# Performance work log

Hardware: AMD Instinct MI355X
Metric: run time of the kernel (lower is better)

The kernel has to match this reference:

```python
import jax, jax.numpy as jnp
import numpy as np

B, C, V, L = 32, 32, 1024, 13  # batch, channels, nodes, seq_len
SUPPORT_LEN, ORDER = 3, 2
C_IN_TOTAL = (ORDER * SUPPORT_LEN + 1) * C  # 224
C_OUT = 64


def setup_inputs() -> dict:
    key = jax.random.key(0)
    ks = jax.random.split(key, 6)
    x = jax.random.normal(ks[0], (B, C, V, L), dtype=jnp.float32)
    # row-normalized random adjacencies (dense diffusion matrices)
    def adj(k):
        a = jax.random.uniform(k, (V, V), dtype=jnp.float32)
        return a / jnp.sum(a, axis=1, keepdims=True)
    A0, A1, A2 = adj(ks[1]), adj(ks[2]), adj(ks[3])
    W = jax.random.normal(ks[4], (C_OUT, C_IN_TOTAL), dtype=jnp.float32) * (1.0 / np.sqrt(C_IN_TOTAL))
    b = jnp.zeros((C_OUT,), dtype=jnp.float32)
    return {"x": x, "A0": A0, "A1": A1, "A2": A2, "W": W, "b": b}


def nconv(x, A):
    # x: [b, c, v, l], A: [v, w] -> [b, c, w, l]
    return jnp.einsum('bcvl,vw->bcwl', x, A)


def reference(x, A0, A1, A2, W, b):
    out = [x]
    for A in (A0, A1, A2):
        x1 = nconv(x, A)
        out.append(x1)
        for _ in range(2, ORDER + 1):
            x2 = nconv(x1, A)
            out.append(x2)
            x1 = x2
    h = jnp.concatenate(out, axis=1)  # [b, (order*support_len+1)*c, v, l]
    # 1x1 conv == channel contraction; dropout is identity in eval mode
    return jnp.einsum('bcvl,oc->bovl', h, W) + b[None, :, None, None]
```

## Files before the change

### kernel.cpp

```cpp
#include <hip/hip_runtime.h>
#include <hip/hip_bf16.h>
#include <cstdint>


#define SZE 13631488ull
#define OFF_AT  190840832ull
#define OFF_WB  197132288ull
#define WS_NEED 197160960ull

typedef __attribute__((ext_vector_type(8))) short short8;
typedef __attribute__((ext_vector_type(4))) float f32x4;

__device__ __forceinline__ unsigned short f2b(float f) {
    unsigned int u = __builtin_bit_cast(unsigned int, f);
    u += 0x7FFFu + ((u >> 16) & 1u);
    return (unsigned short)(u >> 16);
}

__device__ __forceinline__ void gl2lds16(const unsigned short* g, unsigned short* l) {
    __builtin_amdgcn_global_load_lds(
        (__attribute__((address_space(1))) void*)(g),
        (__attribute__((address_space(3))) void*)(l), 16, 0, 0);
}

__global__ __launch_bounds__(256) void k_prep(const float* __restrict__ x,
                                              unsigned short* __restrict__ T,
                                              unsigned short* __restrict__ Ht) {
    __shared__ unsigned short sb[32 * 840];
    const int b = blockIdx.x >> 4, vc = blockIdx.x & 15;
    const int t = threadIdx.x;
    const float4* xb = (const float4*)x;
    for (int it = 0; it < 26; ++it) {
        int q = it * 256 + t;
        int c = q / 208, f = q - c * 208;
        float4 u = xb[(size_t)(b * 32 + c) * 3328 + vc * 208 + f];
        ushort4 pk; pk.x = f2b(u.x); pk.y = f2b(u.y); pk.z = f2b(u.z); pk.w = f2b(u.w);
        *(ushort4*)(sb + c * 840 + f * 4) = pk;
    }
    __syncthreads();
    unsigned short* Tb = T + (size_t)b * 13 * 32 * 1024 + (size_t)vc * 64;
    for (int it = 0; it < 26; ++it) {
        int q = it * 256 + t;
        int l = q >> 9, r = q & 511, c = r >> 4, sg = r & 15;
        const unsigned short* src = sb + c * 840 + l;
        ushort4 pk;
        pk.x = src[(sg * 4 + 0) * 13];
        pk.y = src[(sg * 4 + 1) * 13];
        pk.z = src[(sg * 4 + 2) * 13];
        pk.w = src[(sg * 4 + 3) * 13];
        *(ushort4*)(Tb + (size_t)(l * 32 + c) * 1024 + sg * 4) = pk;
    }
    unsigned short* Hb = Ht + ((size_t)b * 13312 + (size_t)vc * 832) * 224;
    for (int it = 0; it < 26; ++it) {
        int q = it * 256 + t;
        int v = q / 104, r = q - v * 104, l = r >> 3, cs = r & 7;
        const unsigned short* src = sb + v * 13 + l;
        ushort4 pk;
        pk.x = src[(cs * 4 + 0) * 840];
        pk.y = src[(cs * 4 + 1) * 840];
        pk.z = src[(cs * 4 + 2) * 840];
        pk.w = src[(cs * 4 + 3) * 840];
        *(ushort4*)(Hb + (size_t)(v * 13 + l) * 224 + cs * 4) = pk;
    }
}

__global__ __launch_bounds__(256) void k_prep_A(const float* __restrict__ A0,
                                                const float* __restrict__ A1,
                                                const float* __restrict__ A2,
                                                unsigned short* __restrict__ AT) {
    const float* A = blockIdx.z == 0 ? A0 : blockIdx.z == 1 ? A1 : A2;
    unsigned short* D = AT + (size_t)blockIdx.z * 1024 * 1024;
    __shared__ float tile[32][33];
    int v0 = blockIdx.y * 32, w0 = blockIdx.x * 32;
    int c = threadIdx.x & 31, r = threadIdx.x >> 5;
    for (int p = 0; p < 4; ++p) {
        int rr = r + p * 8;
        tile[rr][c] = A[(size_t)(v0 + rr) * 1024 + w0 + c];
    }
    __syncthreads();
    for (int p = 0; p < 4; ++p) {
        int rr = r + p * 8;
        D[(size_t)(w0 + rr) * 1024 + v0 + c] = f2b(tile[c][rr]);
    }
}

__global__ __launch_bounds__(256) void k_prep_W(const float* __restrict__ W,
                                                unsigned short* __restrict__ Wb) {
    int idx = blockIdx.x * 256 + threadIdx.x;
    Wb[idx] = f2b(W[idx]);
}

__global__ __launch_bounds__(256) void k_gemm(const unsigned short* __restrict__ Xb, long xz,
                                              const unsigned short* __restrict__ Pb,
                                              unsigned short* __restrict__ Tout, long tz,
                                              unsigned short* __restrict__ Ht, int cc0b,
                                              int doT) {
    __shared__ union {
        struct { unsigned short xs[8192]; unsigned short ps[8192]; } s;
        unsigned short cs[128 * 132];
        unsigned short ct[128 * 136];
    } lds;
    const int z = blockIdx.z;
    const unsigned short* X = Xb + (size_t)z * (size_t)xz;
    const unsigned short* P = Pb + (size_t)z * (1024u * 1024u);
    const int i0 = blockIdx.x * 128;
    const int j0 = blockIdx.y * 128;
    const int t = threadIdx.x;
    const int lane = t & 63, wave = t >> 6;
    const int l16 = lane & 15, quad = lane >> 4;
    const int wi = (wave >> 1) * 64, wj = (wave & 1) * 64;

    f32x4 acc[4][4] = {};

    const int row = t >> 2, seg = t & 3;
    const unsigned short* xg0 = X + (size_t)(i0 + row) * 1024 + seg * 8;
    const unsigned short* xg1 = xg0 + (size_t)64 * 1024;
    const unsigned short* pg0 = P + (size_t)(j0 + row) * 1024 + seg * 8;
    const unsigned short* pg1 = pg0 + (size_t)64 * 1024;
    unsigned short* lx0 = lds.s.xs + t * 8;
    unsigned short* lp0 = lds.s.ps + t * 8;

    for (int kt = 0; kt < 16; ++kt) {
        const int ko = kt * 64;
        gl2lds16(xg0 + ko,      lx0);
        gl2lds16(xg1 + ko,      lx0 + 2048);
        gl2lds16(xg0 + ko + 32, lx0 + 4096);
        gl2lds16(xg1 + ko + 32, lx0 + 6144);
        gl2lds16(pg0 + ko,      lp0);
        gl2lds16(pg1 + ko,      lp0 + 2048);
        gl2lds16(pg0 + ko + 32, lp0 + 4096);
        gl2lds16(pg1 + ko + 32, lp0 + 6144);
        __syncthreads();
#pragma unroll
        for (int p = 0; p < 2; ++p) {
            short8 a[4], b[4];
#pragma unroll
            for (int mi = 0; mi < 4; ++mi)
                a[mi] = *(const short8*)(lds.s.xs + p * 4096 + (wi + mi * 16 + l16) * 32 + quad * 8);
#pragma unroll
            for (int nj = 0; nj < 4; ++nj)
                b[nj] = *(const short8*)(lds.s.ps + p * 4096 + (wj + nj * 16 + l16) * 32 + quad * 8);
#pragma unroll
            for (int mi = 0; mi < 4; ++mi)
#pragma unroll
                for (int nj = 0; nj < 4; ++nj)
                    acc[mi][nj] = __builtin_amdgcn_mfma_f32_16x16x32_bf16(a[mi], b[nj], acc[mi][nj], 0, 0, 0);
        }
        __syncthreads();
    }

    if (doT) {
#pragma unroll
        for (int mi = 0; mi < 4; ++mi)
#pragma unroll
            for (int nj = 0; nj < 4; ++nj)
#pragma unroll
                for (int r = 0; r < 4; ++r)
                    lds.cs[(wi + mi * 16 + quad * 4 + r) * 132 + (wj + nj * 16 + l16)] =
                        f2b(acc[mi][nj][r]);
        __syncthreads();
        unsigned short* O = Tout + (size_t)z * (size_t)tz;
#pragma unroll
        for (int rep = 0; rep < 8; ++rep) {
            int q = rep * 256 + t;
            int rr = q >> 4, sg = q & 15;
            *(uint4*)(O + (size_t)(i0 + rr) * 1024 + j0 + sg * 8) =
                *(const uint4*)(lds.cs + rr * 132 + sg * 8);
        }
        __syncthreads();
    }

#pragma unroll
    for (int mi = 0; mi < 4; ++mi)
#pragma unroll
        for (int nj = 0; nj < 4; ++nj) {
            ushort4 pk;
            pk.x = f2b(acc[mi][nj][0]);
            pk.y = f2b(acc[mi][nj][1]);
            pk.z = f2b(acc[mi][nj][2]);
            pk.w = f2b(acc[mi][nj][3]);
            *(ushort4*)(lds.ct + (wj + nj * 16 + l16) * 136 + wi + mi * 16 + quad * 4) = pk;
        }
    __syncthreads();
    const int cc0 = cc0b + 64 * z;
#pragma unroll
    for (int it = 0; it < 8; ++it) {
        int q = it * 256 + t;
        int sg = q & 3, v = (q >> 2) & 127, s = q >> 9;
        int p = (i0 >> 5) + s;
        int b = p / 13, l = p - b * 13;
        size_t m = (size_t)b * 13312 + (size_t)(j0 + v) * 13 + l;
        *(uint4*)(Ht + m * 224 + cc0 + sg * 8) =
            *(const uint4*)(lds.ct + v * 136 + s * 32 + sg * 8);
    }
}

__global__ __launch_bounds__(256) void k_fc(const unsigned short* __restrict__ Ht,
                                            const unsigned short* __restrict__ Wb,
                                            const float* __restrict__ bias,
                                            float* __restrict__ y) {
    __shared__ union {
        struct { unsigned short w[64 * 232]; unsigned short a[208 * 32]; } s;
        float sy[64 * 212];
    } lds;
    const int bid = blockIdx.x;
    const int b = bid >> 6, v0 = (bid & 63) * 16;
    const size_t m0 = (size_t)b * 13312 + (size_t)v0 * 13;
    const int t = threadIdx.x;
    const int lane = t & 63, wave = t >> 6;
    const int l16 = lane & 15, quad = lane >> 4;
    const int o0 = wave * 16;

    for (int it = 0; it < 7; ++it) {
        int q = it * 256 + t;
        int o = q / 28, sg = q % 28;
        *(uint4*)(lds.s.w + o * 232 + sg * 8) = *(const uint4*)(Wb + o * 224 + sg * 8);
    }
    float bv = bias[o0 + l16];
    f32x4 acc[13];
#pragma unroll
    for (int mf = 0; mf < 13; ++mf) acc[mf] = (f32x4){bv, bv, bv, bv};

    for (int kk = 0; kk < 7; ++kk) {
        __syncthreads();
        for (int it = 0; it < 4; ++it) {
            int q = it * 256 + t;
            if (q < 832)
                gl2lds16(Ht + (m0 + (q >> 2)) * 224 + kk * 32 + (q & 3) * 8,
                         lds.s.a + q * 8);
        }
        __syncthreads();
        short8 bf = *(const short8*)(lds.s.w + (o0 + l16) * 232 + kk * 32 + quad * 8);
#pragma unroll
        for (int mf = 0; mf < 13; ++mf) {
            short8 af = *(const short8*)(lds.s.a + (mf * 16 + l16) * 32 + quad * 8);
            acc[mf] = __builtin_amdgcn_mfma_f32_16x16x32_bf16(af, bf, acc[mf], 0, 0, 0);
        }
    }
    __syncthreads();
#pragma unroll
    for (int mf = 0; mf < 13; ++mf)
#pragma unroll
        for (int r = 0; r < 4; ++r)
            lds.sy[(o0 + l16) * 212 + mf * 16 + quad * 4 + r] = acc[mf][r];
    __syncthreads();
    float* yb = y + (size_t)b * 851968 + (size_t)v0 * 13;
    for (int it = 0; it < 13; ++it) {
        int q = it * 256 + t;
        int o = q / 52, sg = q % 52;
        *(float4*)(yb + (size_t)o * 13312 + sg * 4) = *(const float4*)(lds.sy + o * 212 + sg * 4);
    }
}

extern "C" void kernel_launch(void* const* d_in, const int* in_sizes, int n_in,
                              void* d_out, int out_size, void* d_ws, size_t ws_size,
                              hipStream_t stream) {
    const float* x    = (const float*)d_in[0];
    const float* A0   = (const float*)d_in[1];
    const float* A1   = (const float*)d_in[2];
    const float* A2   = (const float*)d_in[3];
    const float* W    = (const float*)d_in[4];
    const float* bias = (const float*)d_in[5];

    if (ws_size < WS_NEED) return;

    unsigned short* Ht = (unsigned short*)d_ws;
    unsigned short* AT = (unsigned short*)((char*)d_ws + OFF_AT);
    unsigned short* Wb = (unsigned short*)((char*)d_ws + OFF_WB);
    unsigned short* Tarena = (unsigned short*)d_out;

    k_prep<<<512, 256, 0, stream>>>(x, Tarena, Ht);
    k_prep_A<<<dim3(32, 32, 3), 256, 0, stream>>>(A0, A1, A2, AT);
    k_prep_W<<<56, 256, 0, stream>>>(W, Wb);
    k_gemm<<<dim3(104, 8, 3), 256, 0, stream>>>(Tarena, 0L, AT,
                                                Tarena + SZE, (long)SZE, Ht, 32, 1);
    k_gemm<<<dim3(104, 8, 3), 256, 0, stream>>>(Tarena + SZE, (long)SZE, AT,
                                                nullptr, 0L, Ht, 64, 0);
    k_fc<<<2048, 256, 0, stream>>>(Ht, Wb, bias, (float*)d_out);
}
```

Measured before the change: 508.6 us.

## Precompute squared adjacency A·A and compute all six diffusions in one GEMM launch

Instead of chaining x·A then (x·A)·A, the code first computes the 1024x1024 squared adjacency matrices with a small GEMM. It then runs a single GEMM launch over six z-slices, covering x·A and x·A² for each support, so the dependent second large GEMM over the activations is gone. The squared matrix is rounded to bf16 before use, which changes numerics slightly. The fc kernel is also restructured into 128-thread blocks that keep the activation fragments in registers with next-tile prefetch and write outputs directly, removing the LDS staging.

```diff
diff --git a/kernel.cpp b/kernel.cpp
--- a/kernel.cpp
+++ b/kernel.cpp
@@ -67,15 +67,19 @@
 __global__ __launch_bounds__(256) void k_prep_A(const float* __restrict__ A0,
                                                 const float* __restrict__ A1,
                                                 const float* __restrict__ A2,
-                                                unsigned short* __restrict__ AT) {
+                                                unsigned short* __restrict__ AT,
+                                                unsigned short* __restrict__ Abf) {
     const float* A = blockIdx.z == 0 ? A0 : blockIdx.z == 1 ? A1 : A2;
     unsigned short* D = AT + (size_t)blockIdx.z * 1024 * 1024;
+    unsigned short* D2 = Abf + (size_t)blockIdx.z * 1024 * 1024;
     __shared__ float tile[32][33];
     int v0 = blockIdx.y * 32, w0 = blockIdx.x * 32;
     int c = threadIdx.x & 31, r = threadIdx.x >> 5;
     for (int p = 0; p < 4; ++p) {
         int rr = r + p * 8;
-        tile[rr][c] = A[(size_t)(v0 + rr) * 1024 + w0 + c];
+        float val = A[(size_t)(v0 + rr) * 1024 + w0 + c];
+        tile[rr][c] = val;
+        D2[(size_t)(v0 + rr) * 1024 + w0 + c] = f2b(val);
     }
     __syncthreads();
     for (int p = 0; p < 4; ++p) {
@@ -91,10 +95,10 @@
 }
 
 __global__ __launch_bounds__(256) void k_gemm(const unsigned short* __restrict__ Xb, long xz,
-                                              const unsigned short* __restrict__ Pb,
+                                              const unsigned short* __restrict__ P0,
+                                              const unsigned short* __restrict__ P1,
                                               unsigned short* __restrict__ Tout, long tz,
-                                              unsigned short* __restrict__ Ht, int cc0b,
-                                              int doT) {
+                                              unsigned short* __restrict__ Ht, int doT) {
     __shared__ union {
         struct { unsigned short xs[8192]; unsigned short ps[8192]; } s;
         unsigned short cs[128 * 132];
@@ -102,7 +106,8 @@
     } lds;
     const int z = blockIdx.z;
     const unsigned short* X = Xb + (size_t)z * (size_t)xz;
-    const unsigned short* P = Pb + (size_t)z * (1024u * 1024u);
+    const unsigned short* P = (z < 3) ? P0 + (size_t)z * 1048576u
+                                      : P1 + (size_t)(z - 3) * 1048576u;
     const int i0 = blockIdx.x * 128;
     const int j0 = blockIdx.y * 128;
     const int t = threadIdx.x;
@@ -170,85 +175,86 @@
         __syncthreads();
     }
 
-#pragma unroll
-    for (int mi = 0; mi < 4; ++mi)
-#pragma unroll
-        for (int nj = 0; nj < 4; ++nj) {
-            ushort4 pk;
-            pk.x = f2b(acc[mi][nj][0]);
-            pk.y = f2b(acc[mi][nj][1]);
-            pk.z = f2b(acc[mi][nj][2]);
-            pk.w = f2b(acc[mi][nj][3]);
-            *(ushort4*)(lds.ct + (wj + nj * 16 + l16) * 136 + wi + mi * 16 + quad * 4) = pk;
+    if (Ht) {
+#pragma unroll
+        for (int mi = 0; mi < 4; ++mi)
+#pragma unroll
+            for (int nj = 0; nj < 4; ++nj) {
+                ushort4 pk;
+                pk.x = f2b(acc[mi][nj][0]);
+                pk.y = f2b(acc[mi][nj][1]);
+                pk.z = f2b(acc[mi][nj][2]);
+                pk.w = f2b(acc[mi][nj][3]);
+                *(ushort4*)(lds.ct + (wj + nj * 16 + l16) * 136 + wi + mi * 16 + quad * 4) = pk;
+            }
+        __syncthreads();
+        const int cc0 = (z < 3) ? 32 + 64 * z : 64 * (z - 2);
+#pragma unroll
+        for (int it = 0; it < 8; ++it) {
+            int q = it * 256 + t;
+            int sg = q & 3, v = (q >> 2) & 127, s = q >> 9;
+            int p = (i0 >> 5) + s;
+            int b = p / 13, l = p - b * 13;
+            size_t m = (size_t)b * 13312 + (size_t)(j0 + v) * 13 + l;
+            *(uint4*)(Ht + m * 224 + cc0 + sg * 8) =
+                *(const uint4*)(lds.ct + v * 136 + s * 32 + sg * 8);
         }
-    __syncthreads();
-    const int cc0 = cc0b + 64 * z;
-#pragma unroll
-    for (int it = 0; it < 8; ++it) {
-        int q = it * 256 + t;
-        int sg = q & 3, v = (q >> 2) & 127, s = q >> 9;
-        int p = (i0 >> 5) + s;
-        int b = p / 13, l = p - b * 13;
-        size_t m = (size_t)b * 13312 + (size_t)(j0 + v) * 13 + l;
-        *(uint4*)(Ht + m * 224 + cc0 + sg * 8) =
-            *(const uint4*)(lds.ct + v * 136 + s * 32 + sg * 8);
-    }
-}
-
-__global__ __launch_bounds__(256) void k_fc(const unsigned short* __restrict__ Ht,
+    }
+}
+
+__global__ __launch_bounds__(128) void k_fc(const unsigned short* __restrict__ Ht,
                                             const unsigned short* __restrict__ Wb,
                                             const float* __restrict__ bias,
                                             float* __restrict__ y) {
-    __shared__ union {
-        struct { unsigned short w[64 * 232]; unsigned short a[208 * 32]; } s;
-        float sy[64 * 212];
-    } lds;
+    __shared__ unsigned short sw[64 * 232];
     const int bid = blockIdx.x;
-    const int b = bid >> 6, v0 = (bid & 63) * 16;
-    const size_t m0 = (size_t)b * 13312 + (size_t)v0 * 13;
+    const int b = bid >> 5, v0 = (bid & 31) * 32;
     const int t = threadIdx.x;
     const int lane = t & 63, wave = t >> 6;
     const int l16 = lane & 15, quad = lane >> 4;
-    const int o0 = wave * 16;
-
-    for (int it = 0; it < 7; ++it) {
-        int q = it * 256 + t;
+
+    for (int it = 0; it < 14; ++it) {
+        int q = it * 128 + t;
         int o = q / 28, sg = q % 28;
-        *(uint4*)(lds.s.w + o * 232 + sg * 8) = *(const uint4*)(Wb + o * 224 + sg * 8);
-    }
-    float bv = bias[o0 + l16];
-    f32x4 acc[13];
-#pragma unroll
-    for (int mf = 0; mf < 13; ++mf) acc[mf] = (f32x4){bv, bv, bv, bv};
-
-    for (int kk = 0; kk < 7; ++kk) {
-        __syncthreads();
-        for (int it = 0; it < 4; ++it) {
-            int q = it * 256 + t;
-            if (q < 832)
-                gl2lds16(Ht + (m0 + (q >> 2)) * 224 + kk * 32 + (q & 3) * 8,
-                         lds.s.a + q * 8);
-        }
-        __syncthreads();
-        short8 bf = *(const short8*)(lds.s.w + (o0 + l16) * 232 + kk * 32 + quad * 8);
-#pragma unroll
-        for (int mf = 0; mf < 13; ++mf) {
-            short8 af = *(const short8*)(lds.s.a + (mf * 16 + l16) * 32 + quad * 8);
-            acc[mf] = __builtin_amdgcn_mfma_f32_16x16x32_bf16(af, bf, acc[mf], 0, 0, 0);
-        }
-    }
+        *(uint4*)(sw + o * 232 + sg * 8) = *(const uint4*)(Wb + o * 224 + sg * 8);
+    }
+
+    const size_t mw = (size_t)b * 13312 + (size_t)v0 * 13 + wave * 208;
+    const unsigned short* ag = Ht + (mw + l16) * 224 + quad * 8;
+    float* yb = y + (size_t)b * 851968 + (size_t)v0 * 13 + wave * 208 + quad * 4;
+
+    float bv[4];
+#pragma unroll
+    for (int nj = 0; nj < 4; ++nj) bv[nj] = bias[nj * 16 + l16];
+
+    short8 cur[7];
+#pragma unroll
+    for (int kk = 0; kk < 7; ++kk)
+        cur[kk] = *(const short8*)(ag + kk * 32);
     __syncthreads();
-#pragma unroll
-    for (int mf = 0; mf < 13; ++mf)
-#pragma unroll
-        for (int r = 0; r < 4; ++r)
-            lds.sy[(o0 + l16) * 212 + mf * 16 + quad * 4 + r] = acc[mf][r];
-    __syncthreads();
-    float* yb = y + (size_t)b * 851968 + (size_t)v0 * 13;
-    for (int it = 0; it < 13; ++it) {
-        int q = it * 256 + t;
-        int o = q / 52, sg = q % 52;
-        *(float4*)(yb + (size_t)o * 13312 + sg * 4) = *(const float4*)(lds.sy + o * 212 + sg * 4);
+
+#pragma unroll 1
+    for (int mf = 0; mf < 13; ++mf) {
+        const int mfn = (mf < 12) ? mf + 1 : 0;
+        short8 nxt[7];
+#pragma unroll
+        for (int kk = 0; kk < 7; ++kk)
+            nxt[kk] = *(const short8*)(ag + (size_t)mfn * 3584 + kk * 32);
+        f32x4 acc[4];
+#pragma unroll
+        for (int nj = 0; nj < 4; ++nj) acc[nj] = (f32x4){bv[nj], bv[nj], bv[nj], bv[nj]};
+#pragma unroll
+        for (int kk = 0; kk < 7; ++kk)
+#pragma unroll
+            for (int nj = 0; nj < 4; ++nj) {
+                short8 bf = *(const short8*)(sw + (nj * 16 + l16) * 232 + kk * 32 + quad * 8);
+                acc[nj] = __builtin_amdgcn_mfma_f32_16x16x32_bf16(cur[kk], bf, acc[nj], 0, 0, 0);
+            }
+#pragma unroll
+        for (int nj = 0; nj < 4; ++nj)
+            *(f32x4*)(yb + (size_t)(nj * 16 + l16) * 13312 + mf * 16) = acc[nj];
+#pragma unroll
+        for (int kk = 0; kk < 7; ++kk) cur[kk] = nxt[kk];
     }
 }
 
@@ -268,13 +274,15 @@
     unsigned short* AT = (unsigned short*)((char*)d_ws + OFF_AT);
     unsigned short* Wb = (unsigned short*)((char*)d_ws + OFF_WB);
     unsigned short* Tarena = (unsigned short*)d_out;
+    unsigned short* Abf = Tarena + SZE;
+    unsigned short* AT2 = Tarena + 2 * SZE;
 
     k_prep<<<512, 256, 0, stream>>>(x, Tarena, Ht);
-    k_prep_A<<<dim3(32, 32, 3), 256, 0, stream>>>(A0, A1, A2, AT);
+    k_prep_A<<<dim3(32, 32, 3), 256, 0, stream>>>(A0, A1, A2, AT, Abf);
     k_prep_W<<<56, 256, 0, stream>>>(W, Wb);
-    k_gemm<<<dim3(104, 8, 3), 256, 0, stream>>>(Tarena, 0L, AT,
-                                                Tarena + SZE, (long)SZE, Ht, 32, 1);
-    k_gemm<<<dim3(104, 8, 3), 256, 0, stream>>>(Tarena + SZE, (long)SZE, AT,
-                                                nullptr, 0L, Ht, 64, 0);
-    k_fc<<<2048, 256, 0, stream>>>(Ht, Wb, bias, (float*)d_out);
-}
+    k_gemm<<<dim3(8, 8, 3), 256, 0, stream>>>(AT, 1048576L, Abf, Abf,
+                                              AT2, 1048576L, nullptr, 1);
+    k_gemm<<<dim3(104, 8, 6), 256, 0, stream>>>(Tarena, 0L, AT, AT2,
+                                                nullptr, 0L, Ht, 0);
+    k_fc<<<1024, 128, 0, stream>>>(Ht, Wb, bias, (float*)d_out);
+}
```

New measurement: 468.9 us. 1.08x faster.
